# Optimization experiments

Measured on AMD Instinct MI355X. Metric: run time of the kernel, lower is better.

Reference implementation:

```python
import jax, jax.numpy as jnp
import numpy as np

N = 320      # residues (I == J)
C = 128      # c_in
H = 4        # no_heads
CH = 32      # c_hidden per head
INF = 1.0e9


def setup_inputs() -> dict:
    key = jax.random.key(0)
    ks = jax.random.split(key, 10)
    s = 0.02
    return {
        "x": jax.random.normal(ks[0], (N, N, C), dtype=jnp.float32),
        "mask": jnp.ones((N, N), dtype=jnp.float32),
        "ln_g": jnp.ones((C,), dtype=jnp.float32),
        "ln_b": jnp.zeros((C,), dtype=jnp.float32),
        "w_bias": jax.random.normal(ks[1], (C, H), dtype=jnp.float32) * s,
        "wq": jax.random.normal(ks[2], (C, H * CH), dtype=jnp.float32) * s,
        "wk": jax.random.normal(ks[3], (C, H * CH), dtype=jnp.float32) * s,
        "wv": jax.random.normal(ks[4], (C, H * CH), dtype=jnp.float32) * s,
        "wg": jax.random.normal(ks[5], (C, H * CH), dtype=jnp.float32) * s,
        "bg": jnp.ones((H * CH,), dtype=jnp.float32),  # gating bias init = 1
        "wo": jax.random.normal(ks[6], (H * CH, C), dtype=jnp.float32) * s,
        "bo": jnp.zeros((C,), dtype=jnp.float32),
    }


def _layer_norm(x, g, b, eps=1e-5):
    mu = jnp.mean(x, axis=-1, keepdims=True)
    var = jnp.var(x, axis=-1, keepdims=True)
    return (x - mu) * jax.lax.rsqrt(var + eps) * g + b


def reference(x, mask, ln_g, ln_b, w_bias, wq, wk, wv, wg, bg, wo, bo):
    # starting=True: no transpose
    x = _layer_norm(x, ln_g, ln_b)                       # [I, J, C]
    # mask bias: [I, 1, 1, J]
    mask_bias = (INF * (mask - 1.0))[:, None, None, :]
    # triangle bias: linear(x) -> [I, J, H] -> permute (2,0,1) -> [H, I, J] -> [1, H, I, J]
    tri_bias = jnp.einsum("ijc,ch->hij", x, w_bias)[None]
    # qkv projections (no bias), per-head dim CH; q scaled by 1/sqrt(CH)
    q = jnp.einsum("ijc,cd->ijd", x, wq).reshape(N, N, H, CH) / np.sqrt(CH)
    k = jnp.einsum("ijc,cd->ijd", x, wk).reshape(N, N, H, CH)
    v = jnp.einsum("ijc,cd->ijd", x, wv).reshape(N, N, H, CH)
    # scores over J (per row i): [I, H, J, J]
    scores = jnp.einsum("iqhd,ikhd->ihqk", q, k) + mask_bias + tri_bias
    a = jax.nn.softmax(scores, axis=-1)
    o = jnp.einsum("ihqk,ikhd->iqhd", a, v).reshape(N, N, H * CH)
    g = jax.nn.sigmoid(jnp.einsum("ijc,cd->ijd", x, wg) + bg)
    o = o * g
    return jnp.einsum("ijd,dc->ijc", o, wo) + bo          # [I, J, C]
```

## Files before the change

### kernel.cpp

```cpp
#include <hip/hip_runtime.h>
#include <hip/hip_bf16.h>

#define NN 320
#define CC 128
#define HH 4
#define CHD 32
#define HC 128
#define NP (NN*NN)

typedef __hip_bfloat16 bf16;
typedef __bf16 bfv8 __attribute__((ext_vector_type(8)));
typedef short bsv4 __attribute__((ext_vector_type(4)));
typedef float fv4 __attribute__((ext_vector_type(4)));

__device__ __forceinline__ unsigned short bfbits(float f) {
    bf16 h = __float2bfloat16(f);
    return *reinterpret_cast<unsigned short*>(&h);
}

__device__ __forceinline__ fv4 mfma16x16x16(bsv4 a, bsv4 b, fv4 c) {
    asm("v_mfma_f32_16x16x16_bf16 %0, %1, %2, %0" : "+v"(c) : "v"(a), "v"(b));
    return c;
}

__global__ __launch_bounds__(256) void k_wconv(
    const float* __restrict__ wq, const float* __restrict__ wk,
    const float* __restrict__ wv, const float* __restrict__ wg,
    const float* __restrict__ wo, const float* __restrict__ w_bias,
    bf16* __restrict__ wt, bf16* __restrict__ wot, bf16* __restrict__ wtb)
{
    __shared__ unsigned short T[128 * 136];
    const int b = blockIdx.x, t = threadIdx.x;
    if (b < 5) {
        const float* W = (b == 0) ? wq : (b == 1) ? wk : (b == 2) ? wv : (b == 3) ? wg : wo;
        bf16* D = (b < 4) ? (wt + b * 16384) : wot;
        const float scale = (b == 0) ? 0.17677669529663687f : 1.0f;
        for (int idx = t; idx < 16384; idx += 256) {
            int c = idx >> 7, out = idx & 127;
            T[out * 136 + c] = bfbits(W[idx] * scale);
        }
        __syncthreads();
        for (int i8 = t; i8 < 2048; i8 += 256) {
            int out = i8 >> 4, c0 = (i8 & 15) * 8;
            uint4 v = *reinterpret_cast<const uint4*>(&T[out * 136 + c0]);
            *reinterpret_cast<uint4*>(D + out * 128 + c0) = v;
        }
    } else {
        int out = t >> 4, c0 = (t & 15) * 8;
        unsigned short vals[8];
#pragma unroll
        for (int j = 0; j < 8; j++)
            vals[j] = (out < 4) ? bfbits(w_bias[(c0 + j) * 4 + out]) : (unsigned short)0;
        *reinterpret_cast<uint4*>(wtb + out * 128 + c0) = *reinterpret_cast<uint4*>(vals);
    }
}

__global__ __launch_bounds__(256) void k_proj(
    const float* __restrict__ x, const float* __restrict__ ln_g, const float* __restrict__ ln_b,
    const bf16* __restrict__ wt, const bf16* __restrict__ wtb, const float* __restrict__ bg,
    bf16* __restrict__ qo, bf16* __restrict__ ko, bf16* __restrict__ vo, bf16* __restrict__ go,
    float* __restrict__ tri)
{
    __shared__ __align__(16) unsigned short A[128 * 136];
    const int t = threadIdx.x;
    const int wv = t >> 6, lane = t & 63, g = lane >> 4, c = lane & 15;
    const size_t pb = (size_t)blockIdx.x * 128;

#pragma unroll
    for (int rnd = 0; rnd < 2; rnd++) {
        const int p = (t >> 2) + rnd * 64, l = t & 3;
        const float* xr = x + (pb + p) * CC + l * 32;
        float4 xv[8];
#pragma unroll
        for (int i = 0; i < 8; i++) xv[i] = reinterpret_cast<const float4*>(xr)[i];
        float s = 0.f, s2 = 0.f;
#pragma unroll
        for (int i = 0; i < 8; i++) {
            s  += xv[i].x + xv[i].y + xv[i].z + xv[i].w;
            s2 += xv[i].x * xv[i].x + xv[i].y * xv[i].y + xv[i].z * xv[i].z + xv[i].w * xv[i].w;
        }
        s  += __shfl_xor(s, 1, 4);  s  += __shfl_xor(s, 2, 4);
        s2 += __shfl_xor(s2, 1, 4); s2 += __shfl_xor(s2, 2, 4);
        float mu = s * (1.f / CC);
        float var = s2 * (1.f / CC) - mu * mu;
        float rstd = rsqrtf(var + 1e-5f);
        const float4* gr = reinterpret_cast<const float4*>(ln_g + l * 32);
        const float4* br = reinterpret_cast<const float4*>(ln_b + l * 32);
#pragma unroll
        for (int i = 0; i < 8; i += 2) {
            float4 g0 = gr[i], g1 = gr[i + 1], b0 = br[i], b1 = br[i + 1];
            uint4 pk;
            pk.x = (unsigned)bfbits((xv[i].x - mu) * rstd * g0.x + b0.x)
                 | ((unsigned)bfbits((xv[i].y - mu) * rstd * g0.y + b0.y) << 16);
            pk.y = (unsigned)bfbits((xv[i].z - mu) * rstd * g0.z + b0.z)
                 | ((unsigned)bfbits((xv[i].w - mu) * rstd * g0.w + b0.w) << 16);
            pk.z = (unsigned)bfbits((xv[i+1].x - mu) * rstd * g1.x + b1.x)
                 | ((unsigned)bfbits((xv[i+1].y - mu) * rstd * g1.y + b1.y) << 16);
            pk.w = (unsigned)bfbits((xv[i+1].z - mu) * rstd * g1.z + b1.z)
                 | ((unsigned)bfbits((xv[i+1].w - mu) * rstd * g1.w + b1.w) << 16);
            *reinterpret_cast<uint4*>(&A[p * 136 + l * 32 + i * 4]) = pk;
        }
    }
    __syncthreads();

    bfv8 bx[2][4];
#pragma unroll
    for (int tile = 0; tile < 2; tile++)
#pragma unroll
        for (int kc = 0; kc < 4; kc++)
            bx[tile][kc] = *reinterpret_cast<const bfv8*>(
                &A[(wv * 32 + tile * 16 + c) * 136 + kc * 32 + 8 * g]);

    fv4 zero = {0.f, 0.f, 0.f, 0.f};

    {
        fv4 at0 = zero, at1 = zero;
#pragma unroll
        for (int kc = 0; kc < 4; kc++) {
            bfv8 bb = *reinterpret_cast<const bfv8*>(wtb + c * 128 + kc * 32 + 8 * g);
            at0 = __builtin_amdgcn_mfma_f32_16x16x32_bf16(bx[0][kc], bb, at0, 0, 0, 0);
            at1 = __builtin_amdgcn_mfma_f32_16x16x32_bf16(bx[1][kc], bb, at1, 0, 0, 0);
        }
        if (c < HH) {
            float4 s0 = {at0[0], at0[1], at0[2], at0[3]};
            float4 s1 = {at1[0], at1[1], at1[2], at1[3]};
            float* tb = tri + (size_t)c * NP + pb + wv * 32 + 4 * g;
            *reinterpret_cast<float4*>(tb)      = s0;
            *reinterpret_cast<float4*>(tb + 16) = s1;
        }
    }

    __syncthreads();

    char* Wl = reinterpret_cast<char*>(A);
    bf16* Os[4] = {qo, ko, vo, go};
#pragma unroll 1
    for (int m = 0; m < 4; m++) {
        const uint4* Ws = reinterpret_cast<const uint4*>(wt + m * 16384);
#pragma unroll
        for (int j = 0; j < 8; j++) {
            int bb = t * 128 + j * 16;
            int bs = bb ^ (((bb >> 8) & 7) << 4);
            *reinterpret_cast<uint4*>(Wl + bs) = Ws[t * 8 + j];
        }
        __syncthreads();

        fv4 acc[2][8];
#pragma unroll
        for (int n = 0; n < 8; n++) { acc[0][n] = zero; acc[1][n] = zero; }
#pragma unroll
        for (int n = 0; n < 8; n++)
#pragma unroll
            for (int kc = 0; kc < 4; kc++) {
                const int row = n * 16 + c;
                const int boff = (row * 256 + kc * 64 + g * 16) ^ ((c & 7) << 4);
                bfv8 bw = *reinterpret_cast<const bfv8*>(Wl + boff);
                acc[0][n] = __builtin_amdgcn_mfma_f32_16x16x32_bf16(bw, bx[0][kc], acc[0][n], 0, 0, 0);
                acc[1][n] = __builtin_amdgcn_mfma_f32_16x16x32_bf16(bw, bx[1][kc], acc[1][n], 0, 0, 0);
            }
        if (m == 3) {
#pragma unroll
            for (int n = 0; n < 8; n++) {
                float4 bgv = *reinterpret_cast<const float4*>(bg + n * 16 + 4 * g);
                float bgs[4] = {bgv.x, bgv.y, bgv.z, bgv.w};
#pragma unroll
                for (int tile = 0; tile < 2; tile++)
#pragma unroll
                    for (int r = 0; r < 4; r++) {
                        float z = acc[tile][n][r] + bgs[r];
                        acc[tile][n][r] = 1.f / (1.f + __expf(-z));
                    }
            }
        }
        bf16* O = Os[m];
#pragma unroll
        for (int tile = 0; tile < 2; tile++)
#pragma unroll
            for (int n = 0; n < 8; n++) {
                uint2 pk;
                pk.x = (unsigned)bfbits(acc[tile][n][0]) | ((unsigned)bfbits(acc[tile][n][1]) << 16);
                pk.y = (unsigned)bfbits(acc[tile][n][2]) | ((unsigned)bfbits(acc[tile][n][3]) << 16);
                *reinterpret_cast<uint2*>(O + (pb + wv * 32 + tile * 16 + c) * HC + n * 16 + 4 * g) = pk;
            }
        __syncthreads();
    }
}

__global__ __launch_bounds__(256) void k_attn(
    const bf16* __restrict__ qi, const bf16* __restrict__ ki, const bf16* __restrict__ vi,
    const bf16* __restrict__ gi, const float* __restrict__ mask, const float* __restrict__ tri,
    bf16* __restrict__ oo)
{
    __shared__ __align__(16) unsigned VtW[32 * 164];
    __shared__ __align__(16) unsigned Kw[320 * 20];

    const int t = threadIdx.x;
    const int w = t >> 6, lane = t & 63, g = lane >> 4, c = lane & 15;

    const int r_ = blockIdx.x & 7, pos = blockIdx.x >> 3;
    const int qb5 = pos % 5;
    const int ihh = (pos / 5) * 8 + r_;
    const int h = ihh & 3, i = ihh >> 2;
    const int qb = qb5 * 64 + w * 16;
    const size_t rowbase = (size_t)i * NN;

    const float* maskrow = mask + (size_t)i * NN;
    const float* trirow  = tri + (size_t)h * NP + (size_t)(qb + c) * NN;
    const size_t obase   = (rowbase + qb + c) * HC + h * CHD;

    bfv8 bq = *reinterpret_cast<const bfv8*>(qi + (rowbase + qb + c) * HC + h * CHD + 8 * g);
    uint2 gg0 = *reinterpret_cast<const uint2*>(gi + obase + 4 * g);
    uint2 gg1 = *reinterpret_cast<const uint2*>(gi + obase + 16 + 4 * g);

#pragma unroll
    for (int it = 0; it < 5; it++) {
        int idx = it * 256 + t;
        int key = idx >> 2, oct = idx & 3;
        uint4 kv = *reinterpret_cast<const uint4*>(ki + (rowbase + key) * HC + h * CHD + oct * 8);
        *reinterpret_cast<uint4*>(&Kw[key * 20 + oct * 4]) = kv;
    }

#pragma unroll
    for (int it = 0; it < 3; it++) {
        int idx = it * 256 + t;
        if (idx < 640) {
            int kp = idx >> 2, oct = idx & 3, d0 = oct * 8;
            const uint4 va = *reinterpret_cast<const uint4*>(vi + (rowbase + 2 * kp) * HC + h * CHD + d0);
            const uint4 vb = *reinterpret_cast<const uint4*>(vi + (rowbase + 2 * kp + 1) * HC + h * CHD + d0);
            unsigned a4[4] = {va.x, va.y, va.z, va.w};
            unsigned b4[4] = {vb.x, vb.y, vb.z, vb.w};
#pragma unroll
            for (int u2 = 0; u2 < 4; u2++) {
                int d_e = d0 + 2 * u2, d_o = d_e + 1;
                VtW[d_e * 164 + kp] = (a4[u2] & 0xffffu) | ((b4[u2] & 0xffffu) << 16);
                VtW[d_o * 164 + kp] = (a4[u2] >> 16)     | ((b4[u2] >> 16) << 16);
            }
        }
    }

    __syncthreads();

    const unsigned* Vr0 = &VtW[c * 164];
    const unsigned* Vr1 = &VtW[(16 + c) * 164];
    const unsigned* Kl  = &Kw[c * 20 + 4 * g];

    fv4 zero = {0.f, 0.f, 0.f, 0.f};
    fv4 o0 = zero, o1 = zero;
    float m_run = -3.0e38f, sum = 0.f;

#pragma unroll
    for (int ch = 0; ch < 5; ch++) {
        const int kb = ch * 64;

        bfv8 ak[4]; float4 tr[4], mk[4];
#pragma unroll
        for (int tl = 0; tl < 4; tl++) {
            ak[tl] = *reinterpret_cast<const bfv8*>(Kl + (kb + tl * 16) * 20);
            tr[tl] = *reinterpret_cast<const float4*>(trirow + kb + tl * 16 + 4 * g);
            mk[tl] = *reinterpret_cast<const float4*>(maskrow + kb + tl * 16 + 4 * g);
        }

        fv4 sa[4];
#pragma unroll
        for (int tl = 0; tl < 4; tl++)
            sa[tl] = __builtin_amdgcn_mfma_f32_16x16x32_bf16(ak[tl], bq, zero, 0, 0, 0);

        float s[4][4];
#pragma unroll
        for (int tl = 0; tl < 4; tl++) {
            s[tl][0] = sa[tl][0] + tr[tl].x + fmaf(1.0e9f, mk[tl].x, -1.0e9f);
            s[tl][1] = sa[tl][1] + tr[tl].y + fmaf(1.0e9f, mk[tl].y, -1.0e9f);
            s[tl][2] = sa[tl][2] + tr[tl].z + fmaf(1.0e9f, mk[tl].z, -1.0e9f);
            s[tl][3] = sa[tl][3] + tr[tl].w + fmaf(1.0e9f, mk[tl].w, -1.0e9f);
        }

        float m01 = fmaxf(fmaxf(s[0][0], s[0][1]), fmaxf(s[0][2], s[0][3]));
        float m23 = fmaxf(fmaxf(s[1][0], s[1][1]), fmaxf(s[1][2], s[1][3]));
        float m45 = fmaxf(fmaxf(s[2][0], s[2][1]), fmaxf(s[2][2], s[2][3]));
        float m67 = fmaxf(fmaxf(s[3][0], s[3][1]), fmaxf(s[3][2], s[3][3]));
        float mt = fmaxf(fmaxf(m01, m23), fmaxf(m45, m67));
        mt = fmaxf(mt, __shfl_xor(mt, 16, 64));
        mt = fmaxf(mt, __shfl_xor(mt, 32, 64));

        float mnew = fmaxf(m_run, mt);
        float f = __expf(m_run - mnew);
        m_run = mnew;

        float ls = 0.f;
        unsigned pw[4][2];
#pragma unroll
        for (int tl = 0; tl < 4; tl++) {
            float p0 = __expf(s[tl][0] - mnew);
            float p1 = __expf(s[tl][1] - mnew);
            float p2 = __expf(s[tl][2] - mnew);
            float p3 = __expf(s[tl][3] - mnew);
            ls += (p0 + p1) + (p2 + p3);
            pw[tl][0] = (unsigned)bfbits(p0) | ((unsigned)bfbits(p1) << 16);
            pw[tl][1] = (unsigned)bfbits(p2) | ((unsigned)bfbits(p3) << 16);
        }
        sum = sum * f + ls;
#pragma unroll
        for (int r = 0; r < 4; r++) { o0[r] *= f; o1[r] *= f; }

#pragma unroll
        for (int tl = 0; tl < 4; tl++) {
            union { uint2 u; bsv4 v; } a0u, a1u, pku;
            a0u.u = *reinterpret_cast<const uint2*>(Vr0 + (kb + tl * 16) / 2 + 2 * g);
            a1u.u = *reinterpret_cast<const uint2*>(Vr1 + (kb + tl * 16) / 2 + 2 * g);
            pku.u.x = pw[tl][0]; pku.u.y = pw[tl][1];
            o0 = mfma16x16x16(a0u.v, pku.v, o0);
            o1 = mfma16x16x16(a1u.v, pku.v, o1);
        }
    }

    asm volatile("s_nop 7" :::);
    asm volatile("s_nop 7" :::);

    sum += __shfl_xor(sum, 16, 64);
    sum += __shfl_xor(sum, 32, 64);
    float linv = 1.f / sum;

#pragma unroll
    for (int mt2 = 0; mt2 < 2; mt2++) {
        fv4 oc = mt2 ? o1 : o0;
        uint2 gg = mt2 ? gg1 : gg0;
        int d0 = mt2 * 16 + 4 * g;
        float gf0 = __uint_as_float(gg.x << 16);
        float gf1 = __uint_as_float(gg.x & 0xffff0000u);
        float gf2 = __uint_as_float(gg.y << 16);
        float gf3 = __uint_as_float(gg.y & 0xffff0000u);
        uint2 st;
        st.x = (unsigned)bfbits(oc[0] * linv * gf0) | ((unsigned)bfbits(oc[1] * linv * gf1) << 16);
        st.y = (unsigned)bfbits(oc[2] * linv * gf2) | ((unsigned)bfbits(oc[3] * linv * gf3) << 16);
        *reinterpret_cast<uint2*>(oo + obase + d0) = st;
    }
}

__global__ __launch_bounds__(256) void k_out(
    const bf16* __restrict__ oi, const bf16* __restrict__ wot, const float* __restrict__ bo,
    float* __restrict__ outp)
{
    __shared__ __align__(16) char Wl[32768];
    const int t = threadIdx.x;
    const int wv = t >> 6, lane = t & 63, g = lane >> 4, c = lane & 15;
    const size_t pb = (size_t)blockIdx.x * 64;

    bfv8 bx[4];
#pragma unroll
    for (int kc = 0; kc < 4; kc++)
        bx[kc] = *reinterpret_cast<const bfv8*>(oi + (pb + wv * 16 + c) * HC + kc * 32 + 8 * g);

    const uint4* Ws = reinterpret_cast<const uint4*>(wot);
#pragma unroll
    for (int j = 0; j < 8; j++) {
        int bb = t * 128 + j * 16;
        int bs = bb ^ (((bb >> 8) & 7) << 4);
        *reinterpret_cast<uint4*>(Wl + bs) = Ws[t * 8 + j];
    }
    __syncthreads();

    fv4 zero = {0.f, 0.f, 0.f, 0.f};
    fv4 acc[8];
#pragma unroll
    for (int n = 0; n < 8; n++) acc[n] = zero;
#pragma unroll
    for (int n = 0; n < 8; n++)
#pragma unroll
        for (int kc = 0; kc < 4; kc++) {
            const int row = n * 16 + c;
            const int boff = (row * 256 + kc * 64 + g * 16) ^ ((c & 7) << 4);
            bfv8 bw = *reinterpret_cast<const bfv8*>(Wl + boff);
            acc[n] = __builtin_amdgcn_mfma_f32_16x16x32_bf16(bw, bx[kc], acc[n], 0, 0, 0);
        }
#pragma unroll
    for (int n = 0; n < 8; n++) {
        float4 b4 = *reinterpret_cast<const float4*>(bo + n * 16 + 4 * g);
        float4 st;
        st.x = acc[n][0] + b4.x;
        st.y = acc[n][1] + b4.y;
        st.z = acc[n][2] + b4.z;
        st.w = acc[n][3] + b4.w;
        *reinterpret_cast<float4*>(outp + (pb + wv * 16 + c) * CC + n * 16 + 4 * g) = st;
    }
}

extern "C" void kernel_launch(void* const* d_in, const int* in_sizes, int n_in,
                              void* d_out, int out_size, void* d_ws, size_t ws_size,
                              hipStream_t stream) {
    const float* x      = (const float*)d_in[0];
    const float* mask   = (const float*)d_in[1];
    const float* ln_g   = (const float*)d_in[2];
    const float* ln_b   = (const float*)d_in[3];
    const float* w_bias = (const float*)d_in[4];
    const float* wq     = (const float*)d_in[5];
    const float* wk     = (const float*)d_in[6];
    const float* wv     = (const float*)d_in[7];
    const float* wg     = (const float*)d_in[8];
    const float* bg     = (const float*)d_in[9];
    const float* wo     = (const float*)d_in[10];
    const float* bo     = (const float*)d_in[11];
    float* outp = (float*)d_out;

    bf16* qws = (bf16*)d_ws;
    bf16* kws = qws + (size_t)NP*HC;
    bf16* vws = kws + (size_t)NP*HC;
    bf16* gws = vws + (size_t)NP*HC;
    bf16* ows = gws + (size_t)NP*HC;
    float* tri = (float*)(ows + (size_t)NP*HC);
    bf16* wt  = (bf16*)(tri + (size_t)NP*HH);
    bf16* wot = wt + 4 * 16384;
    bf16* wtb = wot + 16384;

    hipLaunchKernelGGL(k_wconv, dim3(6), dim3(256), 0, stream,
                       wq, wk, wv, wg, wo, w_bias, wt, wot, wtb);
    hipLaunchKernelGGL(k_proj, dim3(NP/128), dim3(256), 0, stream,
                       x, ln_g, ln_b, wt, wtb, bg, qws, kws, vws, gws, tri);
    hipLaunchKernelGGL(k_attn, dim3(6400), dim3(256), 0, stream,
                       qws, kws, vws, gws, mask, tri, ows);
    hipLaunchKernelGGL(k_out, dim3(NP/64), dim3(256), 0, stream,
                       ows, wot, bo, outp);
}
```

Measured before the change: 308.3 us.

## Loop all query tiles per block to reuse staged K/V and split softmax chunks

The attention kernel now launches one block per (row, head) and loops over all five query tiles, so the K and V tiles for that row and head are staged into shared memory once instead of five times. The mask row is cached in shared memory, and the triangle-bias loads for the next chunk are prefetched one chunk ahead. The online softmax is replaced by per-chunk maxima and partial outputs that are rescaled and combined at the end, which removes the serial rescale dependency between chunks. In exchange the grid shrinks from 6400 to 1280 blocks and register pressure rises from holding ten partial accumulators, which may reduce occupancy and latency hiding.

```diff
diff --git a/kernel.cpp b/kernel.cpp
--- a/kernel.cpp
+++ b/kernel.cpp
@@ -193,24 +193,15 @@
 {
     __shared__ __align__(16) unsigned VtW[32 * 164];
     __shared__ __align__(16) unsigned Kw[320 * 20];
+    __shared__ __align__(16) float    Mw[320];
 
     const int t = threadIdx.x;
     const int w = t >> 6, lane = t & 63, g = lane >> 4, c = lane & 15;
 
-    const int r_ = blockIdx.x & 7, pos = blockIdx.x >> 3;
-    const int qb5 = pos % 5;
-    const int ihh = (pos / 5) * 8 + r_;
+    const int ihh = blockIdx.x;
     const int h = ihh & 3, i = ihh >> 2;
-    const int qb = qb5 * 64 + w * 16;
     const size_t rowbase = (size_t)i * NN;
-
     const float* maskrow = mask + (size_t)i * NN;
-    const float* trirow  = tri + (size_t)h * NP + (size_t)(qb + c) * NN;
-    const size_t obase   = (rowbase + qb + c) * HC + h * CHD;
-
-    bfv8 bq = *reinterpret_cast<const bfv8*>(qi + (rowbase + qb + c) * HC + h * CHD + 8 * g);
-    uint2 gg0 = *reinterpret_cast<const uint2*>(gi + obase + 4 * g);
-    uint2 gg1 = *reinterpret_cast<const uint2*>(gi + obase + 16 + 4 * g);
 
 #pragma unroll
     for (int it = 0; it < 5; it++) {
@@ -238,101 +229,143 @@
         }
     }
 
+    if (t < 80)
+        reinterpret_cast<float4*>(Mw)[t] = reinterpret_cast<const float4*>(maskrow)[t];
+
     __syncthreads();
 
     const unsigned* Vr0 = &VtW[c * 164];
     const unsigned* Vr1 = &VtW[(16 + c) * 164];
     const unsigned* Kl  = &Kw[c * 20 + 4 * g];
-
     fv4 zero = {0.f, 0.f, 0.f, 0.f};
-    fv4 o0 = zero, o1 = zero;
-    float m_run = -3.0e38f, sum = 0.f;
-
-#pragma unroll
-    for (int ch = 0; ch < 5; ch++) {
-        const int kb = ch * 64;
-
-        bfv8 ak[4]; float4 tr[4], mk[4];
-#pragma unroll
-        for (int tl = 0; tl < 4; tl++) {
-            ak[tl] = *reinterpret_cast<const bfv8*>(Kl + (kb + tl * 16) * 20);
-            tr[tl] = *reinterpret_cast<const float4*>(trirow + kb + tl * 16 + 4 * g);
-            mk[tl] = *reinterpret_cast<const float4*>(maskrow + kb + tl * 16 + 4 * g);
-        }
-
-        fv4 sa[4];
+
+#pragma unroll 1
+    for (int qt = 0; qt < 5; qt++) {
+        const int qb = qt * 64 + w * 16;
+        const float* trirow = tri + (size_t)h * NP + (size_t)(qb + c) * NN;
+        const size_t obase  = (rowbase + qb + c) * HC + h * CHD;
+
+        bfv8 bq = *reinterpret_cast<const bfv8*>(qi + (rowbase + qb + c) * HC + h * CHD + 8 * g);
+        uint2 gg0 = *reinterpret_cast<const uint2*>(gi + obase + 4 * g);
+        uint2 gg1 = *reinterpret_cast<const uint2*>(gi + obase + 16 + 4 * g);
+
+        fv4 oa[5], ob[5];
+        float mch[5], lsch[5];
+
+        float4 trC[4];
 #pragma unroll
         for (int tl = 0; tl < 4; tl++)
-            sa[tl] = __builtin_amdgcn_mfma_f32_16x16x32_bf16(ak[tl], bq, zero, 0, 0, 0);
-
-        float s[4][4];
-#pragma unroll
-        for (int tl = 0; tl < 4; tl++) {
-            s[tl][0] = sa[tl][0] + tr[tl].x + fmaf(1.0e9f, mk[tl].x, -1.0e9f);
-            s[tl][1] = sa[tl][1] + tr[tl].y + fmaf(1.0e9f, mk[tl].y, -1.0e9f);
-            s[tl][2] = sa[tl][2] + tr[tl].z + fmaf(1.0e9f, mk[tl].z, -1.0e9f);
-            s[tl][3] = sa[tl][3] + tr[tl].w + fmaf(1.0e9f, mk[tl].w, -1.0e9f);
-        }
-
-        float m01 = fmaxf(fmaxf(s[0][0], s[0][1]), fmaxf(s[0][2], s[0][3]));
-        float m23 = fmaxf(fmaxf(s[1][0], s[1][1]), fmaxf(s[1][2], s[1][3]));
-        float m45 = fmaxf(fmaxf(s[2][0], s[2][1]), fmaxf(s[2][2], s[2][3]));
-        float m67 = fmaxf(fmaxf(s[3][0], s[3][1]), fmaxf(s[3][2], s[3][3]));
-        float mt = fmaxf(fmaxf(m01, m23), fmaxf(m45, m67));
-        mt = fmaxf(mt, __shfl_xor(mt, 16, 64));
-        mt = fmaxf(mt, __shfl_xor(mt, 32, 64));
-
-        float mnew = fmaxf(m_run, mt);
-        float f = __expf(m_run - mnew);
-        m_run = mnew;
-
-        float ls = 0.f;
-        unsigned pw[4][2];
-#pragma unroll
-        for (int tl = 0; tl < 4; tl++) {
-            float p0 = __expf(s[tl][0] - mnew);
-            float p1 = __expf(s[tl][1] - mnew);
-            float p2 = __expf(s[tl][2] - mnew);
-            float p3 = __expf(s[tl][3] - mnew);
-            ls += (p0 + p1) + (p2 + p3);
-            pw[tl][0] = (unsigned)bfbits(p0) | ((unsigned)bfbits(p1) << 16);
-            pw[tl][1] = (unsigned)bfbits(p2) | ((unsigned)bfbits(p3) << 16);
-        }
-        sum = sum * f + ls;
-#pragma unroll
-        for (int r = 0; r < 4; r++) { o0[r] *= f; o1[r] *= f; }
-
-#pragma unroll
-        for (int tl = 0; tl < 4; tl++) {
-            union { uint2 u; bsv4 v; } a0u, a1u, pku;
-            a0u.u = *reinterpret_cast<const uint2*>(Vr0 + (kb + tl * 16) / 2 + 2 * g);
-            a1u.u = *reinterpret_cast<const uint2*>(Vr1 + (kb + tl * 16) / 2 + 2 * g);
-            pku.u.x = pw[tl][0]; pku.u.y = pw[tl][1];
-            o0 = mfma16x16x16(a0u.v, pku.v, o0);
-            o1 = mfma16x16x16(a1u.v, pku.v, o1);
-        }
-    }
-
-    asm volatile("s_nop 7" :::);
-    asm volatile("s_nop 7" :::);
-
-    sum += __shfl_xor(sum, 16, 64);
-    sum += __shfl_xor(sum, 32, 64);
-    float linv = 1.f / sum;
-
-#pragma unroll
-    for (int mt2 = 0; mt2 < 2; mt2++) {
-        fv4 oc = mt2 ? o1 : o0;
-        uint2 gg = mt2 ? gg1 : gg0;
-        int d0 = mt2 * 16 + 4 * g;
-        float gf0 = __uint_as_float(gg.x << 16);
-        float gf1 = __uint_as_float(gg.x & 0xffff0000u);
-        float gf2 = __uint_as_float(gg.y << 16);
-        float gf3 = __uint_as_float(gg.y & 0xffff0000u);
-        uint2 st;
-        st.x = (unsigned)bfbits(oc[0] * linv * gf0) | ((unsigned)bfbits(oc[1] * linv * gf1) << 16);
-        st.y = (unsigned)bfbits(oc[2] * linv * gf2) | ((unsigned)bfbits(oc[3] * linv * gf3) << 16);
-        *reinterpret_cast<uint2*>(oo + obase + d0) = st;
+            trC[tl] = *reinterpret_cast<const float4*>(trirow + tl * 16 + 4 * g);
+
+#pragma unroll
+        for (int ch = 0; ch < 5; ch++) {
+            const int kb = ch * 64;
+
+            float4 trN[4];
+            if (ch < 4) {
+#pragma unroll
+                for (int tl = 0; tl < 4; tl++)
+                    trN[tl] = *reinterpret_cast<const float4*>(trirow + kb + 64 + tl * 16 + 4 * g);
+            }
+
+            bfv8 ak[4]; float4 mk[4];
+#pragma unroll
+            for (int tl = 0; tl < 4; tl++) {
+                ak[tl] = *reinterpret_cast<const bfv8*>(Kl + (kb + tl * 16) * 20);
+                mk[tl] = *reinterpret_cast<const float4*>(&Mw[kb + tl * 16 + 4 * g]);
+            }
+
+            fv4 sa[4];
+#pragma unroll
+            for (int tl = 0; tl < 4; tl++)
+                sa[tl] = __builtin_amdgcn_mfma_f32_16x16x32_bf16(ak[tl], bq, zero, 0, 0, 0);
+
+            float s[4][4];
+#pragma unroll
+            for (int tl = 0; tl < 4; tl++) {
+                s[tl][0] = sa[tl][0] + trC[tl].x + fmaf(1.0e9f, mk[tl].x, -1.0e9f);
+                s[tl][1] = sa[tl][1] + trC[tl].y + fmaf(1.0e9f, mk[tl].y, -1.0e9f);
+                s[tl][2] = sa[tl][2] + trC[tl].z + fmaf(1.0e9f, mk[tl].z, -1.0e9f);
+                s[tl][3] = sa[tl][3] + trC[tl].w + fmaf(1.0e9f, mk[tl].w, -1.0e9f);
+            }
+
+            float m01 = fmaxf(fmaxf(s[0][0], s[0][1]), fmaxf(s[0][2], s[0][3]));
+            float m23 = fmaxf(fmaxf(s[1][0], s[1][1]), fmaxf(s[1][2], s[1][3]));
+            float m45 = fmaxf(fmaxf(s[2][0], s[2][1]), fmaxf(s[2][2], s[2][3]));
+            float m67 = fmaxf(fmaxf(s[3][0], s[3][1]), fmaxf(s[3][2], s[3][3]));
+            float mt = fmaxf(fmaxf(m01, m23), fmaxf(m45, m67));
+            mt = fmaxf(mt, __shfl_xor(mt, 16, 64));
+            mt = fmaxf(mt, __shfl_xor(mt, 32, 64));
+            mch[ch] = mt;
+
+            float ls = 0.f;
+            unsigned pw[4][2];
+#pragma unroll
+            for (int tl = 0; tl < 4; tl++) {
+                float p0 = __expf(s[tl][0] - mt);
+                float p1 = __expf(s[tl][1] - mt);
+                float p2 = __expf(s[tl][2] - mt);
+                float p3 = __expf(s[tl][3] - mt);
+                ls += (p0 + p1) + (p2 + p3);
+                pw[tl][0] = (unsigned)bfbits(p0) | ((unsigned)bfbits(p1) << 16);
+                pw[tl][1] = (unsigned)bfbits(p2) | ((unsigned)bfbits(p3) << 16);
+            }
+            lsch[ch] = ls;
+
+            fv4 t0 = zero, t1 = zero;
+#pragma unroll
+            for (int tl = 0; tl < 4; tl++) {
+                union { uint2 u; bsv4 v; } a0u, a1u, pku;
+                a0u.u = *reinterpret_cast<const uint2*>(Vr0 + (kb + tl * 16) / 2 + 2 * g);
+                a1u.u = *reinterpret_cast<const uint2*>(Vr1 + (kb + tl * 16) / 2 + 2 * g);
+                pku.u.x = pw[tl][0]; pku.u.y = pw[tl][1];
+                t0 = mfma16x16x16(a0u.v, pku.v, t0);
+                t1 = mfma16x16x16(a1u.v, pku.v, t1);
+            }
+            oa[ch] = t0; ob[ch] = t1;
+
+            if (ch < 4) {
+#pragma unroll
+                for (int tl = 0; tl < 4; tl++) trC[tl] = trN[tl];
+            }
+        }
+
+        float mstar = fmaxf(fmaxf(fmaxf(mch[0], mch[1]), fmaxf(mch[2], mch[3])), mch[4]);
+        float e0 = __expf(mch[0] - mstar);
+        float e1 = __expf(mch[1] - mstar);
+        float e2 = __expf(mch[2] - mstar);
+        float e3 = __expf(mch[3] - mstar);
+        float e4 = __expf(mch[4] - mstar);
+        float sum = lsch[0] * e0 + lsch[1] * e1 + lsch[2] * e2 + lsch[3] * e3 + lsch[4] * e4;
+        sum += __shfl_xor(sum, 16, 64);
+        sum += __shfl_xor(sum, 32, 64);
+        float linv = 1.f / sum;
+
+        asm volatile("s_nop 7\n\ts_nop 7"
+            : "+v"(oa[0]), "+v"(oa[1]), "+v"(oa[2]), "+v"(oa[3]), "+v"(oa[4]),
+              "+v"(ob[0]), "+v"(ob[1]), "+v"(ob[2]), "+v"(ob[3]), "+v"(ob[4]));
+
+        fv4 o0, o1;
+#pragma unroll
+        for (int r = 0; r < 4; r++) {
+            o0[r] = ((oa[0][r] * e0 + oa[1][r] * e1) + (oa[2][r] * e2 + oa[3][r] * e3)) + oa[4][r] * e4;
+            o1[r] = ((ob[0][r] * e0 + ob[1][r] * e1) + (ob[2][r] * e2 + ob[3][r] * e3)) + ob[4][r] * e4;
+        }
+
+#pragma unroll
+        for (int mt2 = 0; mt2 < 2; mt2++) {
+            fv4 oc = mt2 ? o1 : o0;
+            uint2 gg = mt2 ? gg1 : gg0;
+            int d0 = mt2 * 16 + 4 * g;
+            float gf0 = __uint_as_float(gg.x << 16);
+            float gf1 = __uint_as_float(gg.x & 0xffff0000u);
+            float gf2 = __uint_as_float(gg.y << 16);
+            float gf3 = __uint_as_float(gg.y & 0xffff0000u);
+            uint2 st;
+            st.x = (unsigned)bfbits(oc[0] * linv * gf0) | ((unsigned)bfbits(oc[1] * linv * gf1) << 16);
+            st.y = (unsigned)bfbits(oc[2] * linv * gf2) | ((unsigned)bfbits(oc[3] * linv * gf3) << 16);
+            *reinterpret_cast<uint2*>(oo + obase + d0) = st;
+        }
     }
 }
 
@@ -415,7 +448,7 @@
                        wq, wk, wv, wg, wo, w_bias, wt, wot, wtb);
     hipLaunchKernelGGL(k_proj, dim3(NP/128), dim3(256), 0, stream,
                        x, ln_g, ln_b, wt, wtb, bg, qws, kws, vws, gws, tri);
-    hipLaunchKernelGGL(k_attn, dim3(6400), dim3(256), 0, stream,
+    hipLaunchKernelGGL(k_attn, dim3(NN*HH), dim3(256), 0, stream,
                        qws, kws, vws, gws, mask, tri, ows);
     hipLaunchKernelGGL(k_out, dim3(NP/64), dim3(256), 0, stream,
                        ows, wot, bo, outp);
```

Measured after the change: 300.2 us. 2.6% less time.
